# Optimization experiments

Hardware: AMD Instinct MI355X
Metric: run time of the kernel (lower is better)

Reference implementation:

```python
import jax, jax.numpy as jnp
import numpy as np

N_BR, D, SD, RH, MH, UD, NOBS, B = 4, 256, 64, 64, 128, 16, 25, 32768
LN_EPS = 1e-5

def setup_inputs() -> dict:
    key = jax.random.key(0)
    ks = jax.random.split(key, 16)
    meas_in = D + SD
    rnn_in = RH + UD
    return {
        "z_dyn": jax.random.normal(ks[0], (B, D), jnp.float32),
        "z_static": jax.random.normal(ks[1], (B, SD), jnp.float32),
        "dt": jnp.ones((1,), jnp.float32),
        "ut": jax.random.normal(ks[2], (B, UD), jnp.float32),
        "gates": jax.random.normal(ks[3], (N_BR, D), jnp.float32) * 0.1,
        "W1": jax.random.normal(ks[4], (N_BR, MH, meas_in), jnp.float32) * (1.0 / np.sqrt(meas_in)),
        "b1": jnp.zeros((N_BR, MH), jnp.float32),
        "gamma": jnp.ones((N_BR, MH), jnp.float32),
        "beta": jnp.zeros((N_BR, MH), jnp.float32),
        "W2": jax.random.normal(ks[5], (N_BR, RH, MH), jnp.float32) * (1.0 / np.sqrt(MH)),
        "b2": jnp.zeros((N_BR, RH), jnp.float32),
        "lam_real": jnp.zeros((N_BR, RH), jnp.float32),
        "lam_imag": jax.random.normal(ks[6], (N_BR, RH), jnp.float32) * 0.1,
        "Bmat": jax.random.normal(ks[7], (N_BR, RH, rnn_in), jnp.float32) * (1.0 / np.sqrt(rnn_in)),
        "Wout": jax.random.normal(ks[8], (N_BR, D, RH), jnp.float32) * (1.0 / np.sqrt(RH)),
        "C": jax.random.normal(ks[9], (NOBS, D), jnp.float32) * (1.0 / np.sqrt(D)),
        "D": jax.random.normal(ks[10], (NOBS, UD), jnp.float32) * (1.0 / np.sqrt(UD)),
    }

def reference(z_dyn, z_static, dt, ut, gates, W1, b1, gamma, beta, W2, b2,
              lam_real, lam_imag, Bmat, Wout, C, D):
    ut_dt = ut * dt  # [B,u]
    n, Bsz = gates.shape[0], z_dyn.shape[0]
    # spectral gate per branch: [n,B,d]
    zg = z_dyn[None] * jax.nn.sigmoid(gates)[:, None, :]
    zs = jnp.broadcast_to(z_static[None], (n, Bsz, z_static.shape[-1]))
    x = jnp.concatenate([zg, zs], axis=-1)  # [n,B,meas_in]
    # measurement MLP: Linear -> LayerNorm -> GELU -> Linear
    h = jnp.einsum('nbi,nhi->nbh', x, W1) + b1[:, None, :]
    mu = h.mean(-1, keepdims=True)
    var = ((h - mu) ** 2).mean(-1, keepdims=True)
    h = (h - mu) / jnp.sqrt(var + LN_EPS) * gamma[:, None, :] + beta[:, None, :]
    h = jax.nn.gelu(h, approximate=False)
    g = jnp.einsum('nbh,noh->nbo', h, W2) + b2[:, None, :]  # [n,B,rnn_h]
    u_b = jnp.broadcast_to(ut_dt[None], (n, Bsz, ut_dt.shape[-1]))
    inp = jnp.concatenate([g, u_b], axis=-1)  # [n,B,rnn_h+u]
    b_inp = jnp.einsum('nbi,nhi->nbh', inp, Bmat)
    # complex recurrence step from h0 = 0 (as in forward())
    mag = jax.nn.sigmoid(lam_real) * 0.99
    lam_r = mag * jnp.cos(lam_imag)
    lam_i = mag * jnp.sin(lam_imag)
    h0r = jnp.zeros_like(b_inp)
    h0i = jnp.zeros_like(b_inp)
    h_real = h0r * lam_r[:, None, :] - h0i * lam_i[:, None, :] + b_inp
    # output projection per branch, summed over branches
    z_next = jnp.einsum('nbh,ndh->bd', h_real, Wout)
    yt = z_next @ C.T + ut_dt @ D.T
    return (z_next, yt)
```

## Files before the change

### kernel.cpp

```cpp
#include <hip/hip_runtime.h>
#include <hip/hip_bf16.h>

#define B_ROWS 32768
#define LN_EPS 1e-5f

typedef __bf16 bf16;
using bf16x8 = __attribute__((ext_vector_type(8))) __bf16;
using f32x4  = __attribute__((ext_vector_type(4))) float;


__device__ __forceinline__ float gelu_exact(float x) {
  float s = x * 0.70710678118f;
  float a = fabsf(s);
  float t = __builtin_amdgcn_rcpf(fmaf(0.3275911f, a, 1.0f));
  float p = fmaf(fmaf(fmaf(fmaf(1.061405429f, t, -1.453152027f),
                           t, 1.421413741f), t, -0.284496736f), t, 0.254829592f) * t;
  float e = __expf(-s * s);
  float er = fmaf(-p, e, 1.0f);
  er = copysignf(er, s);
  return 0.5f * x * (1.0f + er);
}

__global__ __launch_bounds__(256) void prep_weights1(
    const float* __restrict__ gates, const float* __restrict__ W1,
    const float* __restrict__ Bmat,  const float* __restrict__ W2,
    const float* __restrict__ b2,    const float* __restrict__ Wout,
    const float* __restrict__ Cm,
    bf16* __restrict__ W1sw, float* __restrict__ Mtmp, float* __restrict__ cvec,
    float* __restrict__ CW)
{
  const int stride = gridDim.x * blockDim.x;
  const int id = blockIdx.x * blockDim.x + threadIdx.x;
  for (int o = id; o < 512 * 320; o += stride) {
    int e = o & 7, m = (o >> 3) & 15, q2 = (o >> 7) & 3, rest = o >> 9;
    int kk = rest % 10, G = rest / 10;
    int n = G * 16 + m, k = kk * 32 + q2 * 8 + e;
    float wv = W1[n * 320 + k];
    if (k < 256) {
      float g = gates[(n >> 7) * 256 + k];
      wv *= 1.f / (1.f + __expf(-g));
    }
    W1sw[o] = (bf16)wv;
  }
  for (int i = id; i < 4 * 64 * 128; i += stride) {
    int n = i >> 13, r = (i >> 7) & 63, h = i & 127;
    float s = 0.f;
    for (int j = 0; j < 64; ++j)
      s += Bmat[(n * 64 + r) * 80 + j] * W2[(n * 64 + j) * 128 + h];
    Mtmp[i] = s;
  }
  for (int i = id; i < 256; i += stride) {
    int n = i >> 6, r = i & 63;
    float s = 0.f;
    for (int j = 0; j < 64; ++j)
      s += Bmat[(n * 64 + r) * 80 + j] * b2[n * 64 + j];
    cvec[i] = s;
  }
  for (int i = id; i < 25 * 256; i += stride) {
    int o = i >> 8, nr = i & 255;
    float s = 0.f;
    for (int d = 0; d < 256; ++d)
      s += Cm[o * 256 + d] * Wout[((nr >> 6) * 256 + d) * 64 + (nr & 63)];
    CW[i] = s;
  }
}

__global__ __launch_bounds__(256) void prep_weights2(
    const float* __restrict__ Wout, const float* __restrict__ Bmat,
    const float* __restrict__ Mtmp, const float* __restrict__ cvec,
    const float* __restrict__ CW,   const float* __restrict__ Dm,
    bf16* __restrict__ Psw)
{
  const int stride = gridDim.x * blockDim.x;
  const int id = blockIdx.x * blockDim.x + threadIdx.x;
  for (int o = id; o < 320 * 544; o += stride) {
    int e = o & 7, m = (o >> 3) & 15, q2 = (o >> 7) & 3, rest = o >> 9;
    int kk2 = rest % 17, G2 = rest / 17;
    int dd = G2 * 16 + m, cc = kk2 * 32 + q2 * 8 + e;
    float s = 0.f;
    if (dd < 281) {
      const bool isC = (dd >= 256);
      const int oo = dd - 256;
      if (cc < 512) {
        int n = cc >> 7, h = cc & 127;
        for (int r = 0; r < 64; ++r) {
          float wv = isC ? CW[(oo * 4 + n) * 64 + r] : Wout[(n * 256 + dd) * 64 + r];
          s += wv * Mtmp[(n * 64 + r) * 128 + h];
        }
      } else if (cc < 528) {
        int u = cc - 512;
        for (int n = 0; n < 4; ++n)
          for (int r = 0; r < 64; ++r) {
            float wv = isC ? CW[(oo * 4 + n) * 64 + r] : Wout[(n * 256 + dd) * 64 + r];
            s += wv * Bmat[(n * 64 + r) * 80 + 64 + u];
          }
        if (isC) s += Dm[oo * 16 + u];
      } else if (cc == 528) {
        for (int n = 0; n < 4; ++n)
          for (int r = 0; r < 64; ++r) {
            float wv = isC ? CW[(oo * 4 + n) * 64 + r] : Wout[(n * 256 + dd) * 64 + r];
            s += wv * cvec[n * 64 + r];
          }
      }
    }
    Psw[o] = (bf16)s;
  }
}

__global__ __launch_bounds__(256, 2) void fused_main(
    const float* __restrict__ zdyn, const float* __restrict__ zst,
    const float* __restrict__ ut,   const float* __restrict__ dtp,
    const bf16* __restrict__ W1sw,  const bf16* __restrict__ Psw,
    const float* __restrict__ b1,   const float* __restrict__ gamma,
    const float* __restrict__ beta,
    float* __restrict__ Z, float* __restrict__ yt)
{
  __shared__ __align__(16) bf16 Xs[64 * 320];
  __shared__ __align__(16) bf16 Hc[2 * 64 * 128];
  __shared__ __align__(16) bf16 Ht[64 * 32];
  __shared__ __align__(16) float partS[64 * 4];
  __shared__ __align__(16) float partQ[64 * 4];

  const int t = threadIdx.x;
  const int lane = t & 63, m16 = lane & 15, q = lane >> 4;
  const int w = t >> 6;
  const int rowBase = blockIdx.x * 64;

  #pragma unroll
  for (int a = 0; a < 10; ++a) {
    int g = a * 256 + t;
    int row = g / 40, pos = g - row * 40;
    int kk = pos >> 2, pq = pos & 3;
    int lq = pq ^ ((row >> 1) & 3);
    int col = kk * 32 + lq * 8;
    const float* src = (col < 256) ? &zdyn[(size_t)(rowBase + row) * 256 + col]
                                   : &zst[(size_t)(rowBase + row) * 64 + (col - 256)];
    float4 v0 = *(const float4*)src;
    float4 v1 = *(const float4*)(src + 4);
    bf16x8 o;
    o[0]=(bf16)v0.x; o[1]=(bf16)v0.y; o[2]=(bf16)v0.z; o[3]=(bf16)v0.w;
    o[4]=(bf16)v1.x; o[5]=(bf16)v1.y; o[6]=(bf16)v1.z; o[7]=(bf16)v1.w;
    *(bf16x8*)&Xs[(size_t)((kk * 64 + row) * 4 + pq) * 8] = o;
  }
  {
    const float dtv = dtp[0];
    int r = t >> 2, pq = t & 3;
    int lq = pq ^ ((r >> 1) & 3);
    bf16x8 o;
    #pragma unroll
    for (int e = 0; e < 8; ++e) {
      int ci = lq * 8 + e;
      float v = (ci < 16) ? ut[(size_t)(rowBase + r) * 16 + ci] * dtv
                          : (ci == 16 ? 1.f : 0.f);
      o[e] = (bf16)v;
    }
    *(bf16x8*)&Ht[t * 8] = o;
  }
  __syncthreads();

  f32x4 accZ[4][5];
  #pragma unroll
  for (int i = 0; i < 4; ++i)
    #pragma unroll
    for (int j = 0; j < 5; ++j)
      #pragma unroll
      for (int r = 0; r < 4; ++r) accZ[i][j][r] = 0.f;

  f32x4 acc1[4][2];

  auto ph1_step = [&](int c, int kk) {
    bf16x8 bfr[2];
    #pragma unroll
    for (int j = 0; j < 2; ++j) {
      int G = c * 8 + w * 2 + j;
      bfr[j] = *(const bf16x8*)&W1sw[(size_t)(((G * 10 + kk) * 4 + q) * 16 + m16) * 8];
    }
    bf16x8 af[4];
    #pragma unroll
    for (int i = 0; i < 4; ++i) {
      int row = i * 16 + m16;
      af[i] = *(const bf16x8*)&Xs[(size_t)((kk * 64 + row) * 4 + (q ^ ((row >> 1) & 3))) * 8];
    }
    __builtin_amdgcn_s_setprio(1);
    #pragma unroll
    for (int i = 0; i < 4; ++i)
      #pragma unroll
      for (int j = 0; j < 2; ++j)
        acc1[i][j] = __builtin_amdgcn_mfma_f32_16x16x32_bf16(af[i], bfr[j], acc1[i][j], 0, 0, 0);
    __builtin_amdgcn_s_setprio(0);
  };

  auto ph2_step = [&](int cprev, int tk) {
    const int hb = (cprev & 1) * 8192;
    int kk2 = cprev * 4 + tk;
    bf16x8 af[4], bfr[5];
    #pragma unroll
    for (int i = 0; i < 4; ++i) {
      int row = i * 16 + m16;
      af[i] = *(const bf16x8*)&Hc[hb + ((tk * 64 + row) * 4 + (q ^ ((row >> 1) & 3))) * 8];
    }
    #pragma unroll
    for (int j = 0; j < 5; ++j) {
      int G2 = w * 5 + j;
      bfr[j] = *(const bf16x8*)&Psw[(size_t)(((G2 * 17 + kk2) * 4 + q) * 16 + m16) * 8];
    }
    __builtin_amdgcn_s_setprio(1);
    #pragma unroll
    for (int i = 0; i < 4; ++i)
      #pragma unroll
      for (int j = 0; j < 5; ++j)
        accZ[i][j] = __builtin_amdgcn_mfma_f32_16x16x32_bf16(af[i], bfr[j], accZ[i][j], 0, 0, 0);
    __builtin_amdgcn_s_setprio(0);
  };

  auto ln_block = [&](int c) {
    const int hbuf = (c & 1) * 8192;
    float bbj[2], gmj[2], btj[2];
    #pragma unroll
    for (int j = 0; j < 2; ++j) {
      int col = c * 128 + w * 32 + j * 16 + m16;
      bbj[j] = b1[col]; gmj[j] = gamma[col]; btj[j] = beta[col];
    }
    #pragma unroll
    for (int i = 0; i < 4; ++i)
      #pragma unroll
      for (int j = 0; j < 2; ++j)
        #pragma unroll
        for (int rr = 0; rr < 4; ++rr) acc1[i][j][rr] += bbj[j];

    #pragma unroll
    for (int i = 0; i < 4; ++i)
      #pragma unroll
      for (int rr = 0; rr < 4; ++rr) {
        float a0 = acc1[i][0][rr], a1 = acc1[i][1][rr];
        float s  = a0 + a1;
        float s2 = fmaf(a0, a0, a1 * a1);
        #pragma unroll
        for (int m = 1; m <= 8; m <<= 1) {
          s  += __shfl_xor(s,  m);
          s2 += __shfl_xor(s2, m);
        }
        if (m16 == 0) {
          int row = i * 16 + q * 4 + rr;
          partS[row * 4 + w] = s;
          partQ[row * 4 + w] = s2;
        }
      }
    __syncthreads();

    #pragma unroll
    for (int i = 0; i < 4; ++i) {
      #pragma unroll
      for (int rr = 0; rr < 4; ++rr) {
        int row = i * 16 + q * 4 + rr;
        f32x4 ps  = *(const f32x4*)&partS[row * 4];
        f32x4 pq2 = *(const f32x4*)&partQ[row * 4];
        float mu = (ps[0] + ps[1] + ps[2] + ps[3]) * 0.0078125f;
        float qq = (pq2[0] + pq2[1] + pq2[2] + pq2[3]) * 0.0078125f;
        float rs = rsqrtf(fmaxf(qq - mu * mu, 0.f) + LN_EPS);
        int rsw = (row >> 1) & 3;
        #pragma unroll
        for (int j = 0; j < 2; ++j) {
          float v = (acc1[i][j][rr] - mu) * rs;
          v = fmaf(v, gmj[j], btj[j]);
          int lq2 = (j * 2 + (m16 >> 3)) ^ rsw;
          Hc[hbuf + ((w * 64 + row) * 4 + lq2) * 8 + (m16 & 7)] = (bf16)gelu_exact(v);
        }
      }
    }
    __syncthreads();
  };

  #pragma unroll
  for (int i = 0; i < 4; ++i)
    #pragma unroll
    for (int j = 0; j < 2; ++j)
      #pragma unroll
      for (int r = 0; r < 4; ++r) acc1[i][j][r] = 0.f;
  #pragma unroll
  for (int kk = 0; kk < 10; ++kk) ph1_step(0, kk);
  ln_block(0);

  #pragma unroll 1
  for (int c = 1; c < 4; ++c) {
    #pragma unroll
    for (int i = 0; i < 4; ++i)
      #pragma unroll
      for (int j = 0; j < 2; ++j)
        #pragma unroll
        for (int r = 0; r < 4; ++r) acc1[i][j][r] = 0.f;
    #pragma unroll
    for (int s = 0; s < 10; ++s) {
      ph1_step(c, s);
      if (s % 3 == 0) ph2_step(c - 1, s / 3);
    }
    ln_block(c);
  }

  #pragma unroll
  for (int tk = 0; tk < 4; ++tk) ph2_step(3, tk);

  {
    bf16x8 af[4], bfr[5];
    #pragma unroll
    for (int i = 0; i < 4; ++i) {
      int row = i * 16 + m16;
      af[i] = *(const bf16x8*)&Ht[(row * 4 + (q ^ ((row >> 1) & 3))) * 8];
    }
    #pragma unroll
    for (int j = 0; j < 5; ++j) {
      int G2 = w * 5 + j;
      bfr[j] = *(const bf16x8*)&Psw[(size_t)(((G2 * 17 + 16) * 4 + q) * 16 + m16) * 8];
    }
    __builtin_amdgcn_s_setprio(1);
    #pragma unroll
    for (int i = 0; i < 4; ++i)
      #pragma unroll
      for (int j = 0; j < 5; ++j)
        accZ[i][j] = __builtin_amdgcn_mfma_f32_16x16x32_bf16(af[i], bfr[j], accZ[i][j], 0, 0, 0);
    __builtin_amdgcn_s_setprio(0);
  }

  #pragma unroll
  for (int i = 0; i < 4; ++i)
    #pragma unroll
    for (int j = 0; j < 5; ++j) {
      int col = w * 80 + j * 16 + m16;
      #pragma unroll
      for (int rr = 0; rr < 4; ++rr) {
        int row = rowBase + i * 16 + q * 4 + rr;
        if (col < 256) Z[(size_t)row * 256 + col] = accZ[i][j][rr];
        else if (col < 281) yt[(size_t)row * 25 + (col - 256)] = accZ[i][j][rr];
      }
    }
}

extern "C" void kernel_launch(void* const* d_in, const int* in_sizes, int n_in,
                              void* d_out, int out_size, void* d_ws, size_t ws_size,
                              hipStream_t stream) {
  const float* zdyn  = (const float*)d_in[0];
  const float* zst   = (const float*)d_in[1];
  const float* dtp   = (const float*)d_in[2];
  const float* ut    = (const float*)d_in[3];
  const float* gates = (const float*)d_in[4];
  const float* W1    = (const float*)d_in[5];
  const float* b1    = (const float*)d_in[6];
  const float* gamma = (const float*)d_in[7];
  const float* beta  = (const float*)d_in[8];
  const float* W2    = (const float*)d_in[9];
  const float* b2    = (const float*)d_in[10];
  const float* Bmat  = (const float*)d_in[13];
  const float* Wout  = (const float*)d_in[14];
  const float* Cm    = (const float*)d_in[15];
  const float* Dm    = (const float*)d_in[16];

  char* ws = (char*)d_ws;
  bf16*  W1sw = (bf16*)(ws);
  bf16*  Psw  = (bf16*)(ws + 327680);
  float* Mtmp = (float*)(ws + 675840);
  float* cvec = (float*)(ws + 806912);
  float* CW   = (float*)(ws + 807936);

  float* Z  = (float*)d_out;
  float* yt = Z + (size_t)B_ROWS * 256;

  hipLaunchKernelGGL(prep_weights1, dim3(256), dim3(256), 0, stream,
                     gates, W1, Bmat, W2, b2, Wout, Cm, W1sw, Mtmp, cvec, CW);
  hipLaunchKernelGGL(prep_weights2, dim3(512), dim3(256), 0, stream,
                     Wout, Bmat, Mtmp, cvec, CW, Dm, Psw);
  hipLaunchKernelGGL(fused_main, dim3(512), dim3(256), 0, stream,
                     zdyn, zst, ut, dtp, W1sw, Psw, b1, gamma, beta, Z, yt);
}
```

Measured before the change: 200.4 us.

## Transpose prep-weight intermediates and vectorize weight-folding dot products

Stores the folded Bmat·W2 product and the Bmat input-column slice transposed so each prep_weights2 dot product reads two contiguous 64-float rows with float4 loads. Vectorizes the W1 gating/bf16 swizzle to 8-wide loads and stores. Also halves the prep kernel grid sizes. The goal is to cut the strided, scalar global reads in the per-call weight preprocessing, which runs alongside the main fused kernel.

```diff
diff --git a/kernel.cpp b/kernel.cpp
--- a/kernel.cpp
+++ b/kernel.cpp
@@ -21,41 +21,65 @@
   return 0.5f * x * (1.0f + er);
 }
 
+__device__ __forceinline__ float dot64(const float* __restrict__ a,
+                                       const float* __restrict__ b) {
+  const f32x4* A = (const f32x4*)a;
+  const f32x4* B = (const f32x4*)b;
+  f32x4 acc = {0.f, 0.f, 0.f, 0.f};
+  #pragma unroll
+  for (int i = 0; i < 16; ++i) acc += A[i] * B[i];
+  return acc[0] + acc[1] + acc[2] + acc[3];
+}
+
 __global__ __launch_bounds__(256) void prep_weights1(
     const float* __restrict__ gates, const float* __restrict__ W1,
     const float* __restrict__ Bmat,  const float* __restrict__ W2,
     const float* __restrict__ b2,    const float* __restrict__ Wout,
     const float* __restrict__ Cm,
-    bf16* __restrict__ W1sw, float* __restrict__ Mtmp, float* __restrict__ cvec,
-    float* __restrict__ CW)
+    bf16* __restrict__ W1sw, float* __restrict__ MtmpT, float* __restrict__ cvec,
+    float* __restrict__ CW,  float* __restrict__ BuT)
 {
   const int stride = gridDim.x * blockDim.x;
   const int id = blockIdx.x * blockDim.x + threadIdx.x;
-  for (int o = id; o < 512 * 320; o += stride) {
-    int e = o & 7, m = (o >> 3) & 15, q2 = (o >> 7) & 3, rest = o >> 9;
+
+  for (int i = id; i < (512 * 320) / 8; i += stride) {
+    int m = i & 15, q2 = (i >> 4) & 3, rest = i >> 6;
     int kk = rest % 10, G = rest / 10;
-    int n = G * 16 + m, k = kk * 32 + q2 * 8 + e;
-    float wv = W1[n * 320 + k];
-    if (k < 256) {
-      float g = gates[(n >> 7) * 256 + k];
-      wv *= 1.f / (1.f + __expf(-g));
-    }
-    W1sw[o] = (bf16)wv;
-  }
+    int n = G * 16 + m, kb = kk * 32 + q2 * 8;
+    float4 v0 = *(const float4*)&W1[n * 320 + kb];
+    float4 v1 = *(const float4*)&W1[n * 320 + kb + 4];
+    float vv[8] = {v0.x, v0.y, v0.z, v0.w, v1.x, v1.y, v1.z, v1.w};
+    if (kb < 256) {
+      float4 g0 = *(const float4*)&gates[(n >> 7) * 256 + kb];
+      float4 g1 = *(const float4*)&gates[(n >> 7) * 256 + kb + 4];
+      float gg[8] = {g0.x, g0.y, g0.z, g0.w, g1.x, g1.y, g1.z, g1.w};
+      #pragma unroll
+      for (int e = 0; e < 8; ++e) vv[e] *= 1.f / (1.f + __expf(-gg[e]));
+    }
+    bf16x8 o;
+    #pragma unroll
+    for (int e = 0; e < 8; ++e) o[e] = (bf16)vv[e];
+    *(bf16x8*)&W1sw[i * 8] = o;
+  }
+
   for (int i = id; i < 4 * 64 * 128; i += stride) {
     int n = i >> 13, r = (i >> 7) & 63, h = i & 127;
     float s = 0.f;
     for (int j = 0; j < 64; ++j)
       s += Bmat[(n * 64 + r) * 80 + j] * W2[(n * 64 + j) * 128 + h];
-    Mtmp[i] = s;
-  }
+    MtmpT[(n * 128 + h) * 64 + r] = s;
+  }
+
   for (int i = id; i < 256; i += stride) {
     int n = i >> 6, r = i & 63;
-    float s = 0.f;
-    for (int j = 0; j < 64; ++j)
-      s += Bmat[(n * 64 + r) * 80 + j] * b2[n * 64 + j];
-    cvec[i] = s;
-  }
+    cvec[i] = dot64(&Bmat[(n * 64 + r) * 80], &b2[n * 64]);
+  }
+
+  for (int i = id; i < 4 * 16 * 64; i += stride) {
+    int n = i >> 10, u = (i >> 6) & 15, r = i & 63;
+    BuT[i] = Bmat[(n * 64 + r) * 80 + 64 + u];
+  }
+
   for (int i = id; i < 25 * 256; i += stride) {
     int o = i >> 8, nr = i & 255;
     float s = 0.f;
@@ -66,9 +90,9 @@
 }
 
 __global__ __launch_bounds__(256) void prep_weights2(
-    const float* __restrict__ Wout, const float* __restrict__ Bmat,
-    const float* __restrict__ Mtmp, const float* __restrict__ cvec,
-    const float* __restrict__ CW,   const float* __restrict__ Dm,
+    const float* __restrict__ Wout, const float* __restrict__ MtmpT,
+    const float* __restrict__ cvec, const float* __restrict__ CW,
+    const float* __restrict__ Dm,   const float* __restrict__ BuT,
     bf16* __restrict__ Psw)
 {
   const int stride = gridDim.x * blockDim.x;
@@ -83,24 +107,22 @@
       const int oo = dd - 256;
       if (cc < 512) {
         int n = cc >> 7, h = cc & 127;
-        for (int r = 0; r < 64; ++r) {
-          float wv = isC ? CW[(oo * 4 + n) * 64 + r] : Wout[(n * 256 + dd) * 64 + r];
-          s += wv * Mtmp[(n * 64 + r) * 128 + h];
-        }
+        const float* a = isC ? &CW[(oo * 4 + n) * 64] : &Wout[(n * 256 + dd) * 64];
+        s = dot64(a, &MtmpT[(n * 128 + h) * 64]);
       } else if (cc < 528) {
         int u = cc - 512;
-        for (int n = 0; n < 4; ++n)
-          for (int r = 0; r < 64; ++r) {
-            float wv = isC ? CW[(oo * 4 + n) * 64 + r] : Wout[(n * 256 + dd) * 64 + r];
-            s += wv * Bmat[(n * 64 + r) * 80 + 64 + u];
-          }
+        #pragma unroll
+        for (int n = 0; n < 4; ++n) {
+          const float* a = isC ? &CW[(oo * 4 + n) * 64] : &Wout[(n * 256 + dd) * 64];
+          s += dot64(a, &BuT[(n * 16 + u) * 64]);
+        }
         if (isC) s += Dm[oo * 16 + u];
       } else if (cc == 528) {
-        for (int n = 0; n < 4; ++n)
-          for (int r = 0; r < 64; ++r) {
-            float wv = isC ? CW[(oo * 4 + n) * 64 + r] : Wout[(n * 256 + dd) * 64 + r];
-            s += wv * cvec[n * 64 + r];
-          }
+        #pragma unroll
+        for (int n = 0; n < 4; ++n) {
+          const float* a = isC ? &CW[(oo * 4 + n) * 64] : &Wout[(n * 256 + dd) * 64];
+          s += dot64(a, &cvec[n * 64]);
+        }
       }
     }
     Psw[o] = (bf16)s;
@@ -355,19 +377,20 @@
   const float* Dm    = (const float*)d_in[16];
 
   char* ws = (char*)d_ws;
-  bf16*  W1sw = (bf16*)(ws);
-  bf16*  Psw  = (bf16*)(ws + 327680);
-  float* Mtmp = (float*)(ws + 675840);
-  float* cvec = (float*)(ws + 806912);
-  float* CW   = (float*)(ws + 807936);
+  bf16*  W1sw  = (bf16*)(ws);
+  bf16*  Psw   = (bf16*)(ws + 327680);
+  float* MtmpT = (float*)(ws + 675840);
+  float* cvec  = (float*)(ws + 806912);
+  float* CW    = (float*)(ws + 807936);
+  float* BuT   = (float*)(ws + 833536);
 
   float* Z  = (float*)d_out;
   float* yt = Z + (size_t)B_ROWS * 256;
 
-  hipLaunchKernelGGL(prep_weights1, dim3(256), dim3(256), 0, stream,
-                     gates, W1, Bmat, W2, b2, Wout, Cm, W1sw, Mtmp, cvec, CW);
-  hipLaunchKernelGGL(prep_weights2, dim3(512), dim3(256), 0, stream,
-                     Wout, Bmat, Mtmp, cvec, CW, Dm, Psw);
+  hipLaunchKernelGGL(prep_weights1, dim3(128), dim3(256), 0, stream,
+                     gates, W1, Bmat, W2, b2, Wout, Cm, W1sw, MtmpT, cvec, CW, BuT);
+  hipLaunchKernelGGL(prep_weights2, dim3(256), dim3(256), 0, stream,
+                     Wout, MtmpT, cvec, CW, Dm, BuT, Psw);
   hipLaunchKernelGGL(fused_main, dim3(512), dim3(256), 0, stream,
                      zdyn, zst, ut, dtp, W1sw, Psw, b1, gamma, beta, Z, yt);
 }
```

After: 202.4 us. Within noise of the previous version (+1.0%).
